# Kernel optimization log

Measured on AMD Instinct MI355X. Metric: run time of the kernel, lower is better.

Reference implementation:

```python
import jax, jax.numpy as jnp
import numpy as np

S = 192          # spatial_size
N = 100000       # active input sites
CIN, M, M2, NCLS = 3, 32, 64, 50
EPS = 1e-4       # scn BatchNorm eps
OFFS = np.array([[dx, dy, dz] for dx in (-1, 0, 1) for dy in (-1, 0, 1) for dz in (-1, 0, 1)], dtype=np.int64)


def _build_nbr(coords, size):
    # coords: [n,3] unique int64. Returns [n,27] int32 neighbor index (-1 = inactive site),
    # i.e. the submanifold-convolution rulebook built via sorted-key hashing.
    n = coords.shape[0]
    keys = (coords[:, 0] * size + coords[:, 1]) * size + coords[:, 2]
    order = np.argsort(keys)
    sk = keys[order]
    nbr = np.full((n, 27), -1, dtype=np.int32)
    for k, off in enumerate(OFFS):
        nc = coords + off
        ok = np.all((nc >= 0) & (nc < size), axis=1)
        qk = (nc[:, 0] * size + nc[:, 1]) * size + nc[:, 2]
        pos = np.searchsorted(sk, qk).clip(0, n - 1)
        hit = ok & (sk[pos] == qk)
        nbr[hit, k] = order[pos[hit]].astype(np.int32)
    return nbr


def setup_inputs() -> dict:
    rng = np.random.default_rng(0)
    raw = rng.integers(0, S, size=(130000, 3), dtype=np.int64)
    keys = (raw[:, 0] * S + raw[:, 1]) * S + raw[:, 2]
    _, first = np.unique(keys, return_index=True)
    coords = raw[np.sort(first)][:N]          # N unique active voxels
    nbr_fine = _build_nbr(coords, S)
    # stride-2 / filter-2 downsample rulebook: coarse sites = unique(coords // 2)
    S2 = S // 2
    cc = coords // 2
    ckeys = (cc[:, 0] * S2 + cc[:, 1]) * S2 + cc[:, 2]
    uk, parent = np.unique(ckeys, return_inverse=True)
    ccoords = np.column_stack((uk // (S2 * S2), (uk // S2) % S2, uk % S2))
    nbr_coarse = _build_nbr(ccoords, S2)
    offset_id = (coords[:, 0] % 2) * 4 + (coords[:, 1] % 2) * 2 + coords[:, 2] % 2
    key = jax.random.key(0)
    ks = jax.random.split(key, 8)
    def w(k, shape, fan):
        return jax.random.normal(k, shape, jnp.float32) * (1.0 / np.sqrt(fan))
    return dict(
        coords=jnp.asarray(coords, jnp.int32),
        features=jax.random.normal(ks[0], (N, CIN), jnp.float32),
        nbr_fine=jnp.asarray(nbr_fine),
        nbr_coarse=jnp.asarray(nbr_coarse),
        parent=jnp.asarray(parent.astype(np.int32)),
        offset_id=jnp.asarray(offset_id.astype(np.int32)),
        num_coarse=int(uk.shape[0]),
        w_in=w(ks[1], (27, CIN, M), 27 * CIN),
        w_b1=w(ks[2], (27, M, M), 27 * M),
        w_down=w(ks[3], (8, M, M2), 8 * M),
        w_b2=w(ks[4], (27, M2, M2), 27 * M2),
        w_up=w(ks[5], (8, M2, M), 8 * M2),
        w_b3=w(ks[6], (27, 2 * M, M), 27 * 2 * M),
        g1=jnp.ones((M,)), b1=jnp.zeros((M,)),
        gd=jnp.ones((M,)), bd=jnp.zeros((M,)),
        g2=jnp.ones((M2,)), b2=jnp.zeros((M2,)),
        gu=jnp.ones((M2,)), bu=jnp.zeros((M2,)),
        g3=jnp.ones((2 * M,)), b3=jnp.zeros((2 * M,)),
        go=jnp.ones((M,)), bo=jnp.zeros((M,)),
        w_lin=w(ks[7], (M, NCLS), M),
        b_lin=jnp.zeros((NCLS,)),
    )


def _subm_conv(f, nbr, W):
    # f: [n,Cin], nbr: [n,27] (-1 = inactive), W: [27,Cin,Cout]
    mask = nbr >= 0
    g = f[jnp.where(mask, nbr, 0)] * mask[..., None]  # [n,27,Cin]
    return jnp.einsum('nkc,kcd->nd', g, W)


def _bnrelu(f, gamma, beta):
    mu = f.mean(0)
    var = ((f - mu) ** 2).mean(0)
    return jax.nn.relu((f - mu) * (gamma / jnp.sqrt(var + EPS)) + beta)


def _down(f, parent, off_id, W, nc):
    # strided 2^3 conv: out[parent] += W[offset(child)] @ f[child]
    out = jnp.zeros((nc, W.shape[2]), f.dtype)
    for o in range(8):
        sel = (off_id == o)[:, None].astype(f.dtype)
        out = out + jax.ops.segment_sum((f * sel) @ W[o], parent, num_segments=nc)
    return out


def _up(g, parent, off_id, W):
    # 2^3 deconv back to fine sites
    gp = g[parent]
    out = jnp.zeros((gp.shape[0], W.shape[2]), g.dtype)
    for o in range(8):
        out = out + (off_id == o)[:, None].astype(g.dtype) * (gp @ W[o])
    return out


def reference(coords, features, nbr_fine, nbr_coarse, parent, offset_id, num_coarse,
              w_in, w_b1, w_down, w_b2, w_up, w_b3,
              g1, b1, gd, bd, g2, b2, gu, bu, g3, b3, go, bo, w_lin, b_lin):
    # InputLayer (coords unique -> identity) + SubmanifoldConvolution(CIN->M)
    f = _subm_conv(features, nbr_fine, w_in)
    # UNet level 0 block (pre-activation)
    f = _subm_conv(_bnrelu(f, g1, b1), nbr_fine, w_b1)
    skip = f
    # downsample: BNReLU + Convolution(M->M2, 2, 2)
    g = _down(_bnrelu(f, gd, bd), parent, offset_id, w_down, num_coarse)
    # UNet level 1 block
    g = _subm_conv(_bnrelu(g, g2, b2), nbr_coarse, w_b2)
    # upsample: BNReLU + Deconvolution(M2->M, 2, 2)
    u = _up(_bnrelu(g, gu, bu), parent, offset_id, w_up)
    # JoinTable + block (2M -> M)
    f = jnp.concatenate([skip, u], axis=1)
    f = _subm_conv(_bnrelu(f, g3, b3), nbr_fine, w_b3)
    # top-level BatchNormReLU(M) + OutputLayer + Linear head
    f = _bnrelu(f, go, bo)
    return f @ w_lin + b_lin
```

## Files before the change

### kernel.cpp

```cpp
#include <hip/hip_runtime.h>

#define EPS_BN 1e-4f
constexpr int BLK = 256;
constexpr int NCOPY = 8;

__global__ __launch_bounds__(64) void build_fine_k(
    const int* __restrict__ nbr, int n, int* __restrict__ cnt, int* __restrict__ ent) {
  int i = blockIdx.x * 64 + threadIdx.x;
  if (i >= n) return;
  int c = 0;
  const int* nr = nbr + (size_t)i * 27;
  int* er = ent + (size_t)i * 27;
#pragma unroll 1
  for (int k = 0; k < 27; ++k) {
    int j = nr[k];
    if (j >= 0) er[c++] = (k << 18) | j;
  }
  cnt[i] = c;
}

__global__ __launch_bounds__(BLK) void child_scatter_k(
    const int* __restrict__ parent, const int* __restrict__ offid, int n,
    int* __restrict__ ccnt, int* __restrict__ cent) {
  int i = blockIdx.x * BLK + threadIdx.x;
  if (i >= n) return;
  int p = parent[i];
  int slot = atomicAdd(&ccnt[p], 1);
  cent[p * 8 + slot] = i | (offid[i] << 25);
}

__global__ __launch_bounds__(BLK) void kcount_k(
    const int* __restrict__ nbr, int n, int* __restrict__ kcnt) {
  __shared__ int lc[27];
  int t = threadIdx.x;
  if (t < 27) lc[t] = 0;
  __syncthreads();
  int i = blockIdx.x * BLK + t;
  if (i < n) {
#pragma unroll 1
    for (int k = 0; k < 27; ++k)
      if (nbr[(size_t)i * 27 + k] >= 0) atomicAdd(&lc[k], 1);
  }
  __syncthreads();
  if (t < 27 && lc[t]) atomicAdd(&kcnt[t], lc[t]);
}

__global__ void kprefix_k(const int* __restrict__ kcnt,
                          int* __restrict__ segSt, int* __restrict__ kfill) {
  if (threadIdx.x == 0) {
    int s = 0;
#pragma unroll 1
    for (int k = 0; k < 27; ++k) {
      segSt[k] = s; kfill[k] = s;
      s += (kcnt[k] + 127) & ~127;
    }
    segSt[27] = s;
  }
}

__global__ __launch_bounds__(BLK) void kscatter_k(
    const int* __restrict__ nbr, int n, int* __restrict__ kfill,
    int* __restrict__ entJ, int* __restrict__ cntC, int* __restrict__ posC) {
  __shared__ int lc[27], lbase[27];
  int t = threadIdx.x;
  if (t < 27) lc[t] = 0;
  __syncthreads();
  int i = blockIdx.x * BLK + t;
  int c = 0;
  if (i < n) {
#pragma unroll 1
    for (int k = 0; k < 27; ++k) {
      if (nbr[(size_t)i * 27 + k] >= 0) { atomicAdd(&lc[k], 1); ++c; }
    }
  }
  __syncthreads();
  if (t < 27) {
    lbase[t] = lc[t] ? atomicAdd(&kfill[t], lc[t]) : 0;
    lc[t] = 0;
  }
  __syncthreads();
  if (i < n) {
    int e = 0;
#pragma unroll 1
    for (int k = 0; k < 27; ++k) {
      int j = nbr[(size_t)i * 27 + k];
      if (j >= 0) {
        int pos = lbase[k] + atomicAdd(&lc[k], 1);
        entJ[pos] = j;
        posC[(size_t)i * 27 + e] = pos;
        ++e;
      }
    }
    cntC[i] = c;
  }
}

__device__ __forceinline__ unsigned f2bf(float x) {
  unsigned u = __float_as_uint(x);
  return (u + 0x7FFFu + ((u >> 16) & 1u)) >> 16;
}

__global__ __launch_bounds__(128) void pgemm_k(
    const float* __restrict__ in, const int* __restrict__ segSt,
    const int* __restrict__ entJ,
    const float* __restrict__ sums, const float* __restrict__ gm,
    const float* __restrict__ bt, float invn,
    const float* __restrict__ W, unsigned short* __restrict__ partials) {
  __shared__ float lw[4096];
  __shared__ float lx[128 * 68];
  __shared__ float lst[128];
  int t = threadIdx.x;
  int base = blockIdx.x * 128;
  if (base >= segSt[27]) return;
  int k = 0;
#pragma unroll 1
  while (segSt[k + 1] <= base) ++k;
  if (t < 64) {
    float s = 0.f, q = 0.f;
#pragma unroll
    for (int cp = 0; cp < NCOPY; ++cp) { s += sums[cp * 128 + t]; q += sums[cp * 128 + 64 + t]; }
    float mu = s * invn, var = q * invn - mu * mu;
    float sc = gm[t] / sqrtf(var + EPS_BN);
    lst[t] = sc; lst[64 + t] = bt[t] - mu * sc;
  }
  const float4* wsrc = reinterpret_cast<const float4*>(W + (size_t)k * 4096);
#pragma unroll
  for (int q = 0; q < 8; ++q)
    reinterpret_cast<float4*>(lw)[t + q * 128] = wsrc[t + q * 128];
  __syncthreads();
#pragma unroll 1
  for (int it = 0; it < 16; ++it) {
    int idx = t + it * 128;
    int pr = idx >> 4, cq = idx & 15;
    int j = entJ[base + pr];
    float4 x = *reinterpret_cast<const float4*>(in + (size_t)j * 64 + cq * 4);
    int cb = cq * 4;
    float y0 = fmaf(x.x, lst[cb + 0], lst[64 + cb + 0]);
    float y1 = fmaf(x.y, lst[cb + 1], lst[64 + cb + 1]);
    float y2 = fmaf(x.z, lst[cb + 2], lst[64 + cb + 2]);
    float y3 = fmaf(x.w, lst[cb + 3], lst[64 + cb + 3]);
    *reinterpret_cast<float4*>(&lx[pr * 68 + cb]) =
        make_float4(y0 > 0.f ? y0 : 0.f, y1 > 0.f ? y1 : 0.f,
                    y2 > 0.f ? y2 : 0.f, y3 > 0.f ? y3 : 0.f);
  }
  __syncthreads();
  int slot = t >> 3, g = (t & 7) * 8;
  float acc[8][8];
#pragma unroll
  for (int pp = 0; pp < 8; ++pp)
#pragma unroll
    for (int b = 0; b < 8; ++b) acc[pp][b] = 0.f;
#pragma unroll
  for (int c4 = 0; c4 < 16; ++c4) {
    int cb = c4 * 4;
    float4 xq[8];
#pragma unroll
    for (int pp = 0; pp < 8; ++pp)
      xq[pp] = *reinterpret_cast<const float4*>(&lx[(slot + 16 * pp) * 68 + cb]);
#pragma unroll
    for (int q = 0; q < 4; ++q) {
      float4 wa = *reinterpret_cast<const float4*>(&lw[(cb + q) * 64 + g]);
      float4 wb = *reinterpret_cast<const float4*>(&lw[(cb + q) * 64 + g + 4]);
      float ws[8] = {wa.x, wa.y, wa.z, wa.w, wb.x, wb.y, wb.z, wb.w};
#pragma unroll
      for (int pp = 0; pp < 8; ++pp) {
        float xv = q == 0 ? xq[pp].x : (q == 1 ? xq[pp].y : (q == 2 ? xq[pp].z : xq[pp].w));
#pragma unroll
        for (int b = 0; b < 8; ++b) acc[pp][b] = fmaf(xv, ws[b], acc[pp][b]);
      }
    }
  }
#pragma unroll
  for (int pp = 0; pp < 8; ++pp) {
    int p = base + slot + 16 * pp;
    uint4 o;
    o.x = f2bf(acc[pp][0]) | (f2bf(acc[pp][1]) << 16);
    o.y = f2bf(acc[pp][2]) | (f2bf(acc[pp][3]) << 16);
    o.z = f2bf(acc[pp][4]) | (f2bf(acc[pp][5]) << 16);
    o.w = f2bf(acc[pp][6]) | (f2bf(acc[pp][7]) << 16);
    *reinterpret_cast<uint4*>(partials + ((size_t)p * 64 + g)) = o;
  }
}

__global__ __launch_bounds__(BLK) void pgather_k(
    const unsigned short* __restrict__ partials, const int* __restrict__ cntC,
    const int* __restrict__ posC, float* __restrict__ out, int nc,
    float* __restrict__ osums) {
  __shared__ float red[256];
  int t = threadIdx.x;
  for (int idx = t; idx < 256; idx += BLK) red[idx] = 0.f;
  __syncthreads();
  int slot = t >> 4, g = (t & 15) * 4;
  int row = blockIdx.x * 16 + slot;
  float a0 = 0.f, a1 = 0.f, a2 = 0.f, a3 = 0.f;
  if (row < nc) {
    int c = cntC[row];
    const int* pr = posC + (size_t)row * 27;
#pragma unroll 1
    for (int e = 0; e < c; ++e) {
      int pos = pr[e];
      uint2 u = *reinterpret_cast<const uint2*>(partials + ((size_t)pos * 64 + g));
      a0 += __uint_as_float(u.x << 16);
      a1 += __uint_as_float(u.x & 0xFFFF0000u);
      a2 += __uint_as_float(u.y << 16);
      a3 += __uint_as_float(u.y & 0xFFFF0000u);
    }
    *reinterpret_cast<float4*>(out + (size_t)row * 64 + g) = make_float4(a0, a1, a2, a3);
  }
  atomicAdd(&red[g + 0], a0); atomicAdd(&red[g + 1], a1);
  atomicAdd(&red[g + 2], a2); atomicAdd(&red[g + 3], a3);
  atomicAdd(&red[128 + g + 0], a0 * a0); atomicAdd(&red[128 + g + 1], a1 * a1);
  atomicAdd(&red[128 + g + 2], a2 * a2); atomicAdd(&red[128 + g + 3], a3 * a3);
  __syncthreads();
  int copy = blockIdx.x & (NCOPY - 1);
  if (t < 128) {
    int half = t >> 6, ch = t & 63;
    atomicAdd(&osums[copy * 128 + half * 64 + ch], red[half * 128 + ch]);
  }
}

template <int CI, int CO, int MODE>
__global__ __launch_bounds__(BLK) void tconvA_k(
    const float* __restrict__ in, const int* __restrict__ ent, const int* __restrict__ cnt,
    const int* __restrict__ parent, const int* __restrict__ offid,
    const float* __restrict__ W, float* __restrict__ out, int n,
    float* __restrict__ osums) {
  constexpr int LANES = CO / 4, SLOTS = BLK / LANES, RPS = 64 / SLOTS;
  __shared__ float red[2 * CO];
  int t = threadIdx.x;
  for (int idx = t; idx < 2 * CO; idx += BLK) red[idx] = 0.f;
  __syncthreads();
  int slot = t / LANES, lane = t % LANES, g = lane * 4;
  int T = blockIdx.x;
  float ssum[4] = {0, 0, 0, 0}, ssq[4] = {0, 0, 0, 0};
#pragma unroll 1
  for (int rr = 0; rr < RPS; ++rr) {
    int row = T * 64 + slot * RPS + rr;
    bool vrow = row < n;
    float a0 = 0.f, a1 = 0.f, a2 = 0.f, a3 = 0.f;
    int ec = 0;
    if (vrow) ec = (MODE == 2) ? 1 : cnt[row];
#pragma unroll 1
    for (int e = 0; e < ec; ++e) {
      int k, j;
      if constexpr (MODE == 0) {
        int v = ent[(size_t)row * 27 + e];
        k = (v >> 18) & 31; j = v & 0x3FFFF;
      } else if constexpr (MODE == 1) {
        int v = ent[(size_t)row * 8 + e];
        k = v >> 25; j = v & 0x1FFFFFF;
      } else {
        k = offid[row]; j = parent[row];
      }
      const float* Wk = W + (size_t)k * (CI * CO) + g;
      const float* xr = in + (size_t)j * CI;
#pragma unroll
      for (int h = 0; h < CI / 32; ++h) {
        float4 xv[8];
#pragma unroll
        for (int c4 = 0; c4 < 8; ++c4)
          xv[c4] = *reinterpret_cast<const float4*>(xr + h * 32 + c4 * 4);
#pragma unroll
        for (int c4 = 0; c4 < 8; ++c4) {
          float xs[4] = {xv[c4].x, xv[c4].y, xv[c4].z, xv[c4].w};
#pragma unroll
          for (int q = 0; q < 4; ++q) {
            float4 wv = *reinterpret_cast<const float4*>(Wk + (size_t)(h * 32 + c4 * 4 + q) * CO);
            a0 = fmaf(xs[q], wv.x, a0);
            a1 = fmaf(xs[q], wv.y, a1);
            a2 = fmaf(xs[q], wv.z, a2);
            a3 = fmaf(xs[q], wv.w, a3);
          }
        }
      }
    }
    if (vrow)
      *reinterpret_cast<float4*>(out + (size_t)row * CO + g) = make_float4(a0, a1, a2, a3);
    ssum[0] += a0; ssum[1] += a1; ssum[2] += a2; ssum[3] += a3;
    ssq[0] = fmaf(a0, a0, ssq[0]); ssq[1] = fmaf(a1, a1, ssq[1]);
    ssq[2] = fmaf(a2, a2, ssq[2]); ssq[3] = fmaf(a3, a3, ssq[3]);
  }
#pragma unroll
  for (int q = 0; q < 4; ++q) {
    atomicAdd(&red[g + q], ssum[q]);
    atomicAdd(&red[CO + g + q], ssq[q]);
  }
  __syncthreads();
  int copy = blockIdx.x & (NCOPY - 1);
  if (t < 2 * CO) atomicAdd(&osums[copy * 2 * CO + t], red[t]);
}

template <int C>
__global__ __launch_bounds__(BLK) void bnact_k(
    const float* __restrict__ in, const float* __restrict__ sums,
    const float* __restrict__ gm, const float* __restrict__ bt, float invn,
    float* __restrict__ outp, int n) {
  __shared__ float lst[2 * C];
  int t = threadIdx.x;
  if (t < C) {
    float s = 0.f, q = 0.f;
#pragma unroll
    for (int cp = 0; cp < NCOPY; ++cp) { s += sums[cp * 2 * C + t]; q += sums[cp * 2 * C + C + t]; }
    float mu = s * invn, var = q * invn - mu * mu;
    float sc = gm[t] / sqrtf(var + EPS_BN);
    lst[t] = sc; lst[C + t] = bt[t] - mu * sc;
  }
  __syncthreads();
  int total = n * (C / 4);
  const float4* in4 = reinterpret_cast<const float4*>(in);
  float4* out4 = reinterpret_cast<float4*>(outp);
  for (int idx = blockIdx.x * BLK + t; idx < total; idx += gridDim.x * BLK) {
    int cb = (idx & (C / 4 - 1)) * 4;
    float4 x = in4[idx];
    float v[4] = {x.x, x.y, x.z, x.w};
#pragma unroll
    for (int q = 0; q < 4; ++q) {
      float y = fmaf(v[q], lst[cb + q], lst[C + cb + q]);
      v[q] = y > 0.f ? y : 0.f;
    }
    out4[idx] = make_float4(v[0], v[1], v[2], v[3]);
  }
}

__global__ __launch_bounds__(BLK) void bncat_k(
    const float* __restrict__ fa, const float* __restrict__ sA,
    const float* __restrict__ gA, const float* __restrict__ bA,
    const float* __restrict__ fb, const float* __restrict__ sB,
    const float* __restrict__ gB, const float* __restrict__ bB,
    float invn, float* __restrict__ acat, int n) {
  __shared__ float lst[128];
  int t = threadIdx.x;
  if (t < 64) {
    int half = t >> 5, c = t & 31;
    const float* ss = half ? sB : sA;
    const float* gg = half ? gB : gA;
    const float* bb = half ? bB : bA;
    float s = 0.f, q = 0.f;
#pragma unroll
    for (int cp = 0; cp < NCOPY; ++cp) { s += ss[cp * 64 + c]; q += ss[cp * 64 + 32 + c]; }
    float mu = s * invn, var = q * invn - mu * mu;
    float sc = gg[c] / sqrtf(var + EPS_BN);
    lst[half * 64 + c] = sc; lst[half * 64 + 32 + c] = bb[c] - mu * sc;
  }
  __syncthreads();
  int total = n * 16;
  for (int idx = blockIdx.x * BLK + t; idx < total; idx += gridDim.x * BLK) {
    int row = idx >> 4, c4 = idx & 15;
    int half = c4 >> 3, cc = (c4 & 7) * 4;
    const float* src = half ? fb : fa;
    float4 x = *reinterpret_cast<const float4*>(src + (size_t)row * 32 + cc);
    const float* L = lst + half * 64;
    float v[4] = {x.x, x.y, x.z, x.w};
#pragma unroll
    for (int q = 0; q < 4; ++q) {
      float y = fmaf(v[q], L[cc + q], L[32 + cc + q]);
      v[q] = y > 0.f ? y : 0.f;
    }
    *reinterpret_cast<float4*>(acat + (size_t)row * 64 + c4 * 4) = make_float4(v[0], v[1], v[2], v[3]);
  }
}

__global__ __launch_bounds__(BLK) void conv_in_k(
    const float* __restrict__ feat, const int* __restrict__ nbr,
    const float* __restrict__ W, float* __restrict__ out, int n,
    float* __restrict__ osums) {
  int i = blockIdx.x * BLK + threadIdx.x;
  bool valid = i < n;
  float acc[32];
#pragma unroll
  for (int c = 0; c < 32; ++c) acc[c] = 0.f;
#pragma unroll 1
  for (int k = 0; k < 27; ++k) {
    int j = valid ? nbr[(size_t)i * 27 + k] : -1;
    if (j < 0) continue;
    float x0 = feat[j * 3 + 0], x1 = feat[j * 3 + 1], x2 = feat[j * 3 + 2];
    const float* w0 = W + k * 96;
#pragma unroll
    for (int co = 0; co < 8; ++co) {
      float4 a = *reinterpret_cast<const float4*>(w0 + co * 4);
      float4 b = *reinterpret_cast<const float4*>(w0 + 32 + co * 4);
      float4 cc = *reinterpret_cast<const float4*>(w0 + 64 + co * 4);
      acc[4*co+0] = fmaf(x0, a.x, fmaf(x1, b.x, fmaf(x2, cc.x, acc[4*co+0])));
      acc[4*co+1] = fmaf(x0, a.y, fmaf(x1, b.y, fmaf(x2, cc.y, acc[4*co+1])));
      acc[4*co+2] = fmaf(x0, a.z, fmaf(x1, b.z, fmaf(x2, cc.z, acc[4*co+2])));
      acc[4*co+3] = fmaf(x0, a.w, fmaf(x1, b.w, fmaf(x2, cc.w, acc[4*co+3])));
    }
  }
  if (valid) {
    float* o = out + (size_t)i * 32;
#pragma unroll
    for (int co = 0; co < 8; ++co)
      *reinterpret_cast<float4*>(o + co * 4) = make_float4(acc[4*co], acc[4*co+1], acc[4*co+2], acc[4*co+3]);
  }
  __shared__ float red[2][4][32];
  int w = threadIdx.x >> 6;
#pragma unroll
  for (int c = 0; c < 32; ++c) {
    float v = acc[c], q = acc[c] * acc[c];
#pragma unroll
    for (int off = 32; off; off >>= 1) {
      v += __shfl_down(v, off);
      q += __shfl_down(q, off);
    }
    if ((threadIdx.x & 63) == 0) { red[0][w][c] = v; red[1][w][c] = q; }
  }
  __syncthreads();
  if (threadIdx.x < 64) {
    int kind = threadIdx.x >> 5, c = threadIdx.x & 31;
    float s = red[kind][0][c] + red[kind][1][c] + red[kind][2][c] + red[kind][3][c];
    atomicAdd(&osums[(blockIdx.x & (NCOPY - 1)) * 64 + kind * 32 + c], s);
  }
}

__global__ __launch_bounds__(BLK) void head_k(
    const float* __restrict__ fin, const float* __restrict__ sums,
    const float* __restrict__ gm, const float* __restrict__ bt, float inv_n,
    const float* __restrict__ Wl, const float* __restrict__ bl,
    float* __restrict__ out, int n) {
  __shared__ float lw[32 * 50];
  __shared__ float lb[52];
  __shared__ float lst[64];
  int t = threadIdx.x;
  if (t < 32) {
    float s = 0.f, q = 0.f;
#pragma unroll
    for (int cp = 0; cp < NCOPY; ++cp) { s += sums[cp * 64 + t]; q += sums[cp * 64 + 32 + t]; }
    float mu = s * inv_n, var = q * inv_n - mu * mu;
    float sc = gm[t] / sqrtf(var + EPS_BN);
    lst[t] = sc; lst[32 + t] = bt[t] - mu * sc;
  }
  for (int idx = t; idx < 1600; idx += BLK) lw[idx] = Wl[idx];
  if (t < 50) lb[t] = bl[t];
  __syncthreads();
  int i = blockIdx.x * BLK + t;
  if (i >= n) return;
  float x[32];
  const float* fj = fin + (size_t)i * 32;
#pragma unroll
  for (int c4 = 0; c4 < 8; ++c4) {
    float4 v = *reinterpret_cast<const float4*>(fj + c4 * 4);
    float vs[4] = {v.x, v.y, v.z, v.w};
#pragma unroll
    for (int q = 0; q < 4; ++q) {
      int c = c4 * 4 + q;
      float y = fmaf(vs[q], lst[c], lst[32 + c]);
      x[c] = y > 0.f ? y : 0.f;
    }
  }
  float acc[50];
#pragma unroll
  for (int co = 0; co < 50; ++co) acc[co] = lb[co];
#pragma unroll 4
  for (int c = 0; c < 32; ++c) {
#pragma unroll
    for (int co = 0; co < 50; ++co) acc[co] = fmaf(x[c], lw[c * 50 + co], acc[co]);
  }
  float* o = out + (size_t)i * 50;
#pragma unroll
  for (int co = 0; co < 25; ++co)
    *reinterpret_cast<float2*>(o + co * 2) = make_float2(acc[co * 2], acc[co * 2 + 1]);
}

extern "C" void kernel_launch(void* const* d_in, const int* in_sizes, int n_in,
                              void* d_out, int out_size, void* d_ws, size_t ws_size,
                              hipStream_t stream) {
  const float* feat   = (const float*)d_in[1];
  const int*   nbrF   = (const int*)d_in[2];
  const int*   nbrC   = (const int*)d_in[3];
  const int*   parent = (const int*)d_in[4];
  const int*   offid  = (const int*)d_in[5];
  const float* w_in   = (const float*)d_in[7];
  const float* w_b1   = (const float*)d_in[8];
  const float* w_down = (const float*)d_in[9];
  const float* w_b2   = (const float*)d_in[10];
  const float* w_up   = (const float*)d_in[11];
  const float* w_b3   = (const float*)d_in[12];
  const float* g1v = (const float*)d_in[13], *b1v = (const float*)d_in[14];
  const float* gdv = (const float*)d_in[15], *bdv = (const float*)d_in[16];
  const float* g2v = (const float*)d_in[17], *b2v = (const float*)d_in[18];
  const float* guv = (const float*)d_in[19], *buv = (const float*)d_in[20];
  const float* g3v = (const float*)d_in[21], *b3v = (const float*)d_in[22];
  const float* gov = (const float*)d_in[23], *bov = (const float*)d_in[24];
  const float* w_lin = (const float*)d_in[25];
  const float* b_lin = (const float*)d_in[26];
  float* out = (float*)d_out;

  int N  = in_sizes[4];
  int NC = in_sizes[3] / 27;
  int ntF = (N + 63) / 64, ntC = (NC + 63) / 64;
  int CAPP = ((NC * 9 / 2) / 128 + 28) * 128;

  size_t szF = (size_t)N * 32;
  size_t szG = (size_t)NC * 64;
  size_t SB  = (size_t)N * 64;

  float* ws = (float*)d_ws;
  float* S1 = ws;
  float* S2 = S1 + SB;
  float* S3 = S2 + SB;
  float* S4 = S3 + szF;
  float* S5 = S4 + szF;
  float* sums1 = S5 + szG;
  float* sumsD = sums1 + 8 * 64;
  float* sums2 = sumsD + 8 * 64;
  float* sumsU = sums2 + 8 * 128;
  float* sums4 = sumsU + 8 * 128;
  float* sums5 = sums4 + 8 * 64;
  int* ccnt = (int*)(sums5 + 8 * 64);
  int* cent = ccnt + NC;
  int* cntF = cent + (size_t)NC * 8;
  int* entF = cntF + N;
  int* kcnt = entF + (size_t)N * 27;
  int* segSt = kcnt + 32;
  int* kfill = segSt + 32;
  int* cntC = kfill + 32;
  int* posC = cntC + NC;
  int* entJ = posC + (size_t)NC * 27;
  unsigned short* partials = (unsigned short*)
      (((uintptr_t)(entJ + CAPP) + 15) & ~(uintptr_t)15);

  hipMemsetAsync(sums1, 0, (4096 + NC) * sizeof(float), stream);
  hipMemsetAsync(kcnt, 0, 96 * sizeof(int), stream);
  hipMemsetAsync(entJ, 0, (size_t)CAPP * sizeof(int), stream);

  int gridN = (N + BLK - 1) / BLK;
  int gridC = (NC + BLK - 1) / BLK;
  int agrid = 1024;
  float invN = 1.f / (float)N, invC = 1.f / (float)NC;

  build_fine_k<<<ntF, 64, 0, stream>>>(nbrF, N, cntF, entF);
  child_scatter_k<<<gridN, BLK, 0, stream>>>(parent, offid, N, ccnt, cent);
  kcount_k<<<gridC, BLK, 0, stream>>>(nbrC, NC, kcnt);
  kprefix_k<<<1, 32, 0, stream>>>(kcnt, segSt, kfill);
  kscatter_k<<<gridC, BLK, 0, stream>>>(nbrC, NC, kfill, entJ, cntC, posC);

  conv_in_k<<<gridN, BLK, 0, stream>>>(feat, nbrF, w_in, S1, N, sums1);
  bnact_k<32><<<agrid, BLK, 0, stream>>>(S1, sums1, g1v, b1v, invN, S2, N);

  tconvA_k<32, 32, 0><<<ntF, BLK, 0, stream>>>(
      S2, entF, cntF, nullptr, nullptr, w_b1, S3, N, sumsD);
  bnact_k<32><<<agrid, BLK, 0, stream>>>(S3, sumsD, gdv, bdv, invN, S4, N);

  tconvA_k<32, 64, 1><<<ntC, BLK, 0, stream>>>(
      S4, cent, ccnt, nullptr, nullptr, w_down, S5, NC, sums2);

  int gridP1 = CAPP / 128;
  pgemm_k<<<gridP1, 128, 0, stream>>>(
      S5, segSt, entJ, sums2, g2v, b2v, invC, w_b2, partials);
  pgather_k<<<(NC + 15) / 16, BLK, 0, stream>>>(
      partials, cntC, posC, S1, NC, sumsU);

  bnact_k<64><<<agrid, BLK, 0, stream>>>(S1, sumsU, guv, buv, invC, S5, NC);

  tconvA_k<64, 32, 2><<<ntF, BLK, 0, stream>>>(
      S5, nullptr, nullptr, parent, offid, w_up, S4, N, sums4);

  bncat_k<<<agrid, BLK, 0, stream>>>(
      S3, sumsD, g3v, b3v, S4, sums4, g3v + 32, b3v + 32, invN, S2, N);

  tconvA_k<64, 32, 0><<<ntF, BLK, 0, stream>>>(
      S2, entF, cntF, nullptr, nullptr, w_b3, S3, N, sums5);

  head_k<<<gridN, BLK, 0, stream>>>(S3, sums5, gov, bov, invN, w_lin, b_lin, out, N);
}
```

Measured before the change: 527.4 us.

## Use per-offset gather-GEMM-scatter for fine submanifold convolutions with fused BN and concat

Both fine-level submanifold convolutions (w_b1 and w_b3) now use the offset-grouped rulebook path that previously served only the coarse conv. Entries are grouped by kernel offset, each group runs a dense GEMM against one shared-memory weight slice, and a gather kernel sums fp32 partials per output row. The BN+ReLU that used to run as separate bnact and bncat passes is folded into the GEMM input load, and the concat is read directly from two source buffers. This replaces per-row atomic-style convolution with more reuse of the weights, but adds fine rulebook build kernels and a large fp32 partials round trip.

```diff
diff --git a/kernel.cpp b/kernel.cpp
--- a/kernel.cpp
+++ b/kernel.cpp
@@ -3,21 +3,6 @@
 #define EPS_BN 1e-4f
 constexpr int BLK = 256;
 constexpr int NCOPY = 8;
-
-__global__ __launch_bounds__(64) void build_fine_k(
-    const int* __restrict__ nbr, int n, int* __restrict__ cnt, int* __restrict__ ent) {
-  int i = blockIdx.x * 64 + threadIdx.x;
-  if (i >= n) return;
-  int c = 0;
-  const int* nr = nbr + (size_t)i * 27;
-  int* er = ent + (size_t)i * 27;
-#pragma unroll 1
-  for (int k = 0; k < 27; ++k) {
-    int j = nr[k];
-    if (j >= 0) er[c++] = (k << 18) | j;
-  }
-  cnt[i] = c;
-}
 
 __global__ __launch_bounds__(BLK) void child_scatter_k(
     const int* __restrict__ parent, const int* __restrict__ offid, int n,
@@ -60,7 +45,7 @@
 
 __global__ __launch_bounds__(BLK) void kscatter_k(
     const int* __restrict__ nbr, int n, int* __restrict__ kfill,
-    int* __restrict__ entJ, int* __restrict__ cntC, int* __restrict__ posC) {
+    int* __restrict__ entJ, int* __restrict__ cntR, int* __restrict__ posR) {
   __shared__ int lc[27], lbase[27];
   int t = threadIdx.x;
   if (t < 27) lc[t] = 0;
@@ -69,9 +54,8 @@
   int c = 0;
   if (i < n) {
 #pragma unroll 1
-    for (int k = 0; k < 27; ++k) {
+    for (int k = 0; k < 27; ++k)
       if (nbr[(size_t)i * 27 + k] >= 0) { atomicAdd(&lc[k], 1); ++c; }
-    }
   }
   __syncthreads();
   if (t < 27) {
@@ -87,11 +71,11 @@
       if (j >= 0) {
         int pos = lbase[k] + atomicAdd(&lc[k], 1);
         entJ[pos] = j;
-        posC[(size_t)i * 27 + e] = pos;
+        posR[(size_t)i * 27 + e] = pos;
         ++e;
       }
     }
-    cntC[i] = c;
+    cntR[i] = c;
   }
 }
 
@@ -100,70 +84,88 @@
   return (u + 0x7FFFu + ((u >> 16) & 1u)) >> 16;
 }
 
+template <int CI, int CO, bool CAT, bool BF>
 __global__ __launch_bounds__(128) void pgemm_k(
-    const float* __restrict__ in, const int* __restrict__ segSt,
-    const int* __restrict__ entJ,
-    const float* __restrict__ sums, const float* __restrict__ gm,
-    const float* __restrict__ bt, float invn,
-    const float* __restrict__ W, unsigned short* __restrict__ partials) {
-  __shared__ float lw[4096];
-  __shared__ float lx[128 * 68];
-  __shared__ float lst[128];
+    const float* __restrict__ inA, const float* __restrict__ inB,
+    const int* __restrict__ segSt, const int* __restrict__ entJ,
+    const float* __restrict__ sumsA, const float* __restrict__ gmA,
+    const float* __restrict__ btA, float invA,
+    const float* __restrict__ sumsB, const float* __restrict__ gmB,
+    const float* __restrict__ btB, float invB,
+    const float* __restrict__ W, void* __restrict__ partials) {
+  constexpr int XP = CI + 4;
+  constexpr int C4 = CI / 4;
+  constexpr int NS = 1024 / CO;
+  constexpr int PP = 128 / NS;
+  constexpr int CIA = CAT ? CI / 2 : CI;
+  constexpr int WL = CI * CO / 512;
+  __shared__ float lw[CI * CO];
+  __shared__ float lx[128 * XP];
+  __shared__ float lst[2 * CI];
   int t = threadIdx.x;
   int base = blockIdx.x * 128;
   if (base >= segSt[27]) return;
   int k = 0;
 #pragma unroll 1
   while (segSt[k + 1] <= base) ++k;
-  if (t < 64) {
+  if (t < CI) {
+    const float* S; const float* G; const float* B; float inv; int c;
+    if (!CAT || t < CIA) { S = sumsA; G = gmA; B = btA; inv = invA; c = t; }
+    else { S = sumsB; G = gmB; B = btB; inv = invB; c = t - CIA; }
     float s = 0.f, q = 0.f;
 #pragma unroll
-    for (int cp = 0; cp < NCOPY; ++cp) { s += sums[cp * 128 + t]; q += sums[cp * 128 + 64 + t]; }
-    float mu = s * invn, var = q * invn - mu * mu;
-    float sc = gm[t] / sqrtf(var + EPS_BN);
-    lst[t] = sc; lst[64 + t] = bt[t] - mu * sc;
-  }
-  const float4* wsrc = reinterpret_cast<const float4*>(W + (size_t)k * 4096);
-#pragma unroll
-  for (int q = 0; q < 8; ++q)
+    for (int cp = 0; cp < NCOPY; ++cp) { s += S[cp * 2 * CIA + c]; q += S[cp * 2 * CIA + CIA + c]; }
+    float mu = s * inv, var = q * inv - mu * mu;
+    float sc = G[c] / sqrtf(var + EPS_BN);
+    lst[t] = sc; lst[CI + t] = B[c] - mu * sc;
+  }
+  const float4* wsrc = reinterpret_cast<const float4*>(W + (size_t)k * (CI * CO));
+#pragma unroll
+  for (int q = 0; q < WL; ++q)
     reinterpret_cast<float4*>(lw)[t + q * 128] = wsrc[t + q * 128];
   __syncthreads();
 #pragma unroll 1
-  for (int it = 0; it < 16; ++it) {
+  for (int it = 0; it < C4; ++it) {
     int idx = t + it * 128;
-    int pr = idx >> 4, cq = idx & 15;
+    int pr = idx / C4, cq = idx % C4;
     int j = entJ[base + pr];
-    float4 x = *reinterpret_cast<const float4*>(in + (size_t)j * 64 + cq * 4);
     int cb = cq * 4;
-    float y0 = fmaf(x.x, lst[cb + 0], lst[64 + cb + 0]);
-    float y1 = fmaf(x.y, lst[cb + 1], lst[64 + cb + 1]);
-    float y2 = fmaf(x.z, lst[cb + 2], lst[64 + cb + 2]);
-    float y3 = fmaf(x.w, lst[cb + 3], lst[64 + cb + 3]);
-    *reinterpret_cast<float4*>(&lx[pr * 68 + cb]) =
+    float4 x;
+    if constexpr (CAT) {
+      x = (cb < CIA) ? *reinterpret_cast<const float4*>(inA + (size_t)j * CIA + cb)
+                     : *reinterpret_cast<const float4*>(inB + (size_t)j * CIA + (cb - CIA));
+    } else {
+      x = *reinterpret_cast<const float4*>(inA + (size_t)j * CI + cb);
+    }
+    float y0 = fmaf(x.x, lst[cb + 0], lst[CI + cb + 0]);
+    float y1 = fmaf(x.y, lst[cb + 1], lst[CI + cb + 1]);
+    float y2 = fmaf(x.z, lst[cb + 2], lst[CI + cb + 2]);
+    float y3 = fmaf(x.w, lst[cb + 3], lst[CI + cb + 3]);
+    *reinterpret_cast<float4*>(&lx[pr * XP + cb]) =
         make_float4(y0 > 0.f ? y0 : 0.f, y1 > 0.f ? y1 : 0.f,
                     y2 > 0.f ? y2 : 0.f, y3 > 0.f ? y3 : 0.f);
   }
   __syncthreads();
-  int slot = t >> 3, g = (t & 7) * 8;
-  float acc[8][8];
-#pragma unroll
-  for (int pp = 0; pp < 8; ++pp)
+  int slot = t / PP, g = (t % PP) * 8;
+  float acc[PP][8];
+#pragma unroll
+  for (int pp = 0; pp < PP; ++pp)
 #pragma unroll
     for (int b = 0; b < 8; ++b) acc[pp][b] = 0.f;
 #pragma unroll
-  for (int c4 = 0; c4 < 16; ++c4) {
+  for (int c4 = 0; c4 < C4; ++c4) {
     int cb = c4 * 4;
-    float4 xq[8];
-#pragma unroll
-    for (int pp = 0; pp < 8; ++pp)
-      xq[pp] = *reinterpret_cast<const float4*>(&lx[(slot + 16 * pp) * 68 + cb]);
+    float4 xq[PP];
+#pragma unroll
+    for (int pp = 0; pp < PP; ++pp)
+      xq[pp] = *reinterpret_cast<const float4*>(&lx[(slot + NS * pp) * XP + cb]);
 #pragma unroll
     for (int q = 0; q < 4; ++q) {
-      float4 wa = *reinterpret_cast<const float4*>(&lw[(cb + q) * 64 + g]);
-      float4 wb = *reinterpret_cast<const float4*>(&lw[(cb + q) * 64 + g + 4]);
+      float4 wa = *reinterpret_cast<const float4*>(&lw[(cb + q) * CO + g]);
+      float4 wb = *reinterpret_cast<const float4*>(&lw[(cb + q) * CO + g + 4]);
       float ws[8] = {wa.x, wa.y, wa.z, wa.w, wb.x, wb.y, wb.z, wb.w};
 #pragma unroll
-      for (int pp = 0; pp < 8; ++pp) {
+      for (int pp = 0; pp < PP; ++pp) {
         float xv = q == 0 ? xq[pp].x : (q == 1 ? xq[pp].y : (q == 2 ? xq[pp].z : xq[pp].w));
 #pragma unroll
         for (int b = 0; b < 8; ++b) acc[pp][b] = fmaf(xv, ws[b], acc[pp][b]);
@@ -171,52 +173,62 @@
     }
   }
 #pragma unroll
-  for (int pp = 0; pp < 8; ++pp) {
-    int p = base + slot + 16 * pp;
-    uint4 o;
-    o.x = f2bf(acc[pp][0]) | (f2bf(acc[pp][1]) << 16);
-    o.y = f2bf(acc[pp][2]) | (f2bf(acc[pp][3]) << 16);
-    o.z = f2bf(acc[pp][4]) | (f2bf(acc[pp][5]) << 16);
-    o.w = f2bf(acc[pp][6]) | (f2bf(acc[pp][7]) << 16);
-    *reinterpret_cast<uint4*>(partials + ((size_t)p * 64 + g)) = o;
-  }
-}
-
+  for (int pp = 0; pp < PP; ++pp) {
+    size_t p = base + slot + NS * pp;
+    if constexpr (BF) {
+      uint4 o;
+      o.x = f2bf(acc[pp][0]) | (f2bf(acc[pp][1]) << 16);
+      o.y = f2bf(acc[pp][2]) | (f2bf(acc[pp][3]) << 16);
+      o.z = f2bf(acc[pp][4]) | (f2bf(acc[pp][5]) << 16);
+      o.w = f2bf(acc[pp][6]) | (f2bf(acc[pp][7]) << 16);
+      *reinterpret_cast<uint4*>((unsigned short*)partials + p * CO + g) = o;
+    } else {
+      float* pf = (float*)partials + p * CO + g;
+      *reinterpret_cast<float4*>(pf) = make_float4(acc[pp][0], acc[pp][1], acc[pp][2], acc[pp][3]);
+      *reinterpret_cast<float4*>(pf + 4) = make_float4(acc[pp][4], acc[pp][5], acc[pp][6], acc[pp][7]);
+    }
+  }
+}
+
+template <int CO, bool BF>
 __global__ __launch_bounds__(BLK) void pgather_k(
-    const unsigned short* __restrict__ partials, const int* __restrict__ cntC,
-    const int* __restrict__ posC, float* __restrict__ out, int nc,
+    const void* __restrict__ partials, const int* __restrict__ cntR,
+    const int* __restrict__ posR, float* __restrict__ out, int n,
     float* __restrict__ osums) {
-  __shared__ float red[256];
-  int t = threadIdx.x;
-  for (int idx = t; idx < 256; idx += BLK) red[idx] = 0.f;
-  __syncthreads();
-  int slot = t >> 4, g = (t & 15) * 4;
-  int row = blockIdx.x * 16 + slot;
+  constexpr int LPS = CO / 4, RPB = BLK / LPS;
+  __shared__ float red[2 * CO];
+  int t = threadIdx.x;
+  for (int idx = t; idx < 2 * CO; idx += BLK) red[idx] = 0.f;
+  __syncthreads();
+  int slot = t / LPS, g = (t % LPS) * 4;
+  int row = blockIdx.x * RPB + slot;
   float a0 = 0.f, a1 = 0.f, a2 = 0.f, a3 = 0.f;
-  if (row < nc) {
-    int c = cntC[row];
-    const int* pr = posC + (size_t)row * 27;
+  if (row < n) {
+    int c = cntR[row];
+    const int* pr = posR + (size_t)row * 27;
 #pragma unroll 1
     for (int e = 0; e < c; ++e) {
-      int pos = pr[e];
-      uint2 u = *reinterpret_cast<const uint2*>(partials + ((size_t)pos * 64 + g));
-      a0 += __uint_as_float(u.x << 16);
-      a1 += __uint_as_float(u.x & 0xFFFF0000u);
-      a2 += __uint_as_float(u.y << 16);
-      a3 += __uint_as_float(u.y & 0xFFFF0000u);
-    }
-    *reinterpret_cast<float4*>(out + (size_t)row * 64 + g) = make_float4(a0, a1, a2, a3);
+      size_t pos = (size_t)pr[e];
+      if constexpr (BF) {
+        uint2 u = *reinterpret_cast<const uint2*>((const unsigned short*)partials + pos * CO + g);
+        a0 += __uint_as_float(u.x << 16);
+        a1 += __uint_as_float(u.x & 0xFFFF0000u);
+        a2 += __uint_as_float(u.y << 16);
+        a3 += __uint_as_float(u.y & 0xFFFF0000u);
+      } else {
+        float4 v = *reinterpret_cast<const float4*>((const float*)partials + pos * CO + g);
+        a0 += v.x; a1 += v.y; a2 += v.z; a3 += v.w;
+      }
+    }
+    *reinterpret_cast<float4*>(out + (size_t)row * CO + g) = make_float4(a0, a1, a2, a3);
   }
   atomicAdd(&red[g + 0], a0); atomicAdd(&red[g + 1], a1);
   atomicAdd(&red[g + 2], a2); atomicAdd(&red[g + 3], a3);
-  atomicAdd(&red[128 + g + 0], a0 * a0); atomicAdd(&red[128 + g + 1], a1 * a1);
-  atomicAdd(&red[128 + g + 2], a2 * a2); atomicAdd(&red[128 + g + 3], a3 * a3);
+  atomicAdd(&red[CO + g + 0], a0 * a0); atomicAdd(&red[CO + g + 1], a1 * a1);
+  atomicAdd(&red[CO + g + 2], a2 * a2); atomicAdd(&red[CO + g + 3], a3 * a3);
   __syncthreads();
   int copy = blockIdx.x & (NCOPY - 1);
-  if (t < 128) {
-    int half = t >> 6, ch = t & 63;
-    atomicAdd(&osums[copy * 128 + half * 64 + ch], red[half * 128 + ch]);
-  }
+  if (t < 2 * CO) atomicAdd(&osums[copy * 2 * CO + t], red[t]);
 }
 
 template <int CI, int CO, int MODE>
@@ -243,10 +255,7 @@
 #pragma unroll 1
     for (int e = 0; e < ec; ++e) {
       int k, j;
-      if constexpr (MODE == 0) {
-        int v = ent[(size_t)row * 27 + e];
-        k = (v >> 18) & 31; j = v & 0x3FFFF;
-      } else if constexpr (MODE == 1) {
+      if constexpr (MODE == 1) {
         int v = ent[(size_t)row * 8 + e];
         k = v >> 25; j = v & 0x1FFFFFF;
       } else {
@@ -319,44 +328,6 @@
       v[q] = y > 0.f ? y : 0.f;
     }
     out4[idx] = make_float4(v[0], v[1], v[2], v[3]);
-  }
-}
-
-__global__ __launch_bounds__(BLK) void bncat_k(
-    const float* __restrict__ fa, const float* __restrict__ sA,
-    const float* __restrict__ gA, const float* __restrict__ bA,
-    const float* __restrict__ fb, const float* __restrict__ sB,
-    const float* __restrict__ gB, const float* __restrict__ bB,
-    float invn, float* __restrict__ acat, int n) {
-  __shared__ float lst[128];
-  int t = threadIdx.x;
-  if (t < 64) {
-    int half = t >> 5, c = t & 31;
-    const float* ss = half ? sB : sA;
-    const float* gg = half ? gB : gA;
-    const float* bb = half ? bB : bA;
-    float s = 0.f, q = 0.f;
-#pragma unroll
-    for (int cp = 0; cp < NCOPY; ++cp) { s += ss[cp * 64 + c]; q += ss[cp * 64 + 32 + c]; }
-    float mu = s * invn, var = q * invn - mu * mu;
-    float sc = gg[c] / sqrtf(var + EPS_BN);
-    lst[half * 64 + c] = sc; lst[half * 64 + 32 + c] = bb[c] - mu * sc;
-  }
-  __syncthreads();
-  int total = n * 16;
-  for (int idx = blockIdx.x * BLK + t; idx < total; idx += gridDim.x * BLK) {
-    int row = idx >> 4, c4 = idx & 15;
-    int half = c4 >> 3, cc = (c4 & 7) * 4;
-    const float* src = half ? fb : fa;
-    float4 x = *reinterpret_cast<const float4*>(src + (size_t)row * 32 + cc);
-    const float* L = lst + half * 64;
-    float v[4] = {x.x, x.y, x.z, x.w};
-#pragma unroll
-    for (int q = 0; q < 4; ++q) {
-      float y = fmaf(v[q], L[cc + q], L[32 + cc + q]);
-      v[q] = y > 0.f ? y : 0.f;
-    }
-    *reinterpret_cast<float4*>(acat + (size_t)row * 64 + c4 * 4) = make_float4(v[0], v[1], v[2], v[3]);
   }
 }
 
@@ -488,78 +459,81 @@
   int N  = in_sizes[4];
   int NC = in_sizes[3] / 27;
   int ntF = (N + 63) / 64, ntC = (NC + 63) / 64;
-  int CAPP = ((NC * 9 / 2) / 128 + 28) * 128;
-
-  size_t szF = (size_t)N * 32;
-  size_t szG = (size_t)NC * 64;
-  size_t SB  = (size_t)N * 64;
+  int CAPPF = ((N * 3) / 128 + 28) * 128;
+  int CAPPC = ((NC * 9 / 2) / 128 + 28) * 128;
 
   float* ws = (float*)d_ws;
-  float* S1 = ws;
-  float* S2 = S1 + SB;
-  float* S3 = S2 + SB;
-  float* S4 = S3 + szF;
-  float* S5 = S4 + szF;
-  float* sums1 = S5 + szG;
+  float* B1 = ws;
+  float* B2 = B1 + (size_t)N * 32;
+  float* B3 = B2 + (size_t)N * 32;
+  float* B4 = B3 + (size_t)N * 32;
+  float* B5 = B4 + (size_t)NC * 64;
+  float* sums1 = B5 + (size_t)NC * 64;
   float* sumsD = sums1 + 8 * 64;
   float* sums2 = sumsD + 8 * 64;
   float* sumsU = sums2 + 8 * 128;
   float* sums4 = sumsU + 8 * 128;
   float* sums5 = sums4 + 8 * 64;
   int* ccnt = (int*)(sums5 + 8 * 64);
-  int* cent = ccnt + NC;
+  int* kcntF = ccnt + NC;
+  int* kcntC = kcntF + 32;
+  int* segStF = kcntC + 32;
+  int* kfillF = segStF + 32;
+  int* segStC = kfillF + 32;
+  int* kfillC = segStC + 32;
+  int* cent = kfillC + 32;
   int* cntF = cent + (size_t)NC * 8;
-  int* entF = cntF + N;
-  int* kcnt = entF + (size_t)N * 27;
-  int* segSt = kcnt + 32;
-  int* kfill = segSt + 32;
-  int* cntC = kfill + 32;
+  int* posF = cntF + N;
+  int* cntC = posF + (size_t)N * 27;
   int* posC = cntC + NC;
-  int* entJ = posC + (size_t)NC * 27;
-  unsigned short* partials = (unsigned short*)
-      (((uintptr_t)(entJ + CAPP) + 15) & ~(uintptr_t)15);
-
-  hipMemsetAsync(sums1, 0, (4096 + NC) * sizeof(float), stream);
-  hipMemsetAsync(kcnt, 0, 96 * sizeof(int), stream);
-  hipMemsetAsync(entJ, 0, (size_t)CAPP * sizeof(int), stream);
+  int* entJF = posC + (size_t)NC * 27;
+  int* entJC = entJF + CAPPF;
+  float* partialsF = (float*)(((uintptr_t)(entJC + CAPPC) + 15) & ~(uintptr_t)15);
+  unsigned short* partialsC = (unsigned short*)(partialsF + (size_t)CAPPF * 32);
+
+  hipMemsetAsync(sums1, 0, (4096 + NC + 64) * sizeof(float), stream);
+  hipMemsetAsync(entJF, 0, (size_t)(CAPPF + CAPPC) * sizeof(int), stream);
 
   int gridN = (N + BLK - 1) / BLK;
   int gridC = (NC + BLK - 1) / BLK;
   int agrid = 1024;
   float invN = 1.f / (float)N, invC = 1.f / (float)NC;
 
-  build_fine_k<<<ntF, 64, 0, stream>>>(nbrF, N, cntF, entF);
+  kcount_k<<<gridN, BLK, 0, stream>>>(nbrF, N, kcntF);
+  kcount_k<<<gridC, BLK, 0, stream>>>(nbrC, NC, kcntC);
+  kprefix_k<<<1, 32, 0, stream>>>(kcntF, segStF, kfillF);
+  kprefix_k<<<1, 32, 0, stream>>>(kcntC, segStC, kfillC);
+  kscatter_k<<<gridN, BLK, 0, stream>>>(nbrF, N, kfillF, entJF, cntF, posF);
+  kscatter_k<<<gridC, BLK, 0, stream>>>(nbrC, NC, kfillC, entJC, cntC, posC);
   child_scatter_k<<<gridN, BLK, 0, stream>>>(parent, offid, N, ccnt, cent);
-  kcount_k<<<gridC, BLK, 0, stream>>>(nbrC, NC, kcnt);
-  kprefix_k<<<1, 32, 0, stream>>>(kcnt, segSt, kfill);
-  kscatter_k<<<gridC, BLK, 0, stream>>>(nbrC, NC, kfill, entJ, cntC, posC);
-
-  conv_in_k<<<gridN, BLK, 0, stream>>>(feat, nbrF, w_in, S1, N, sums1);
-  bnact_k<32><<<agrid, BLK, 0, stream>>>(S1, sums1, g1v, b1v, invN, S2, N);
-
-  tconvA_k<32, 32, 0><<<ntF, BLK, 0, stream>>>(
-      S2, entF, cntF, nullptr, nullptr, w_b1, S3, N, sumsD);
-  bnact_k<32><<<agrid, BLK, 0, stream>>>(S3, sumsD, gdv, bdv, invN, S4, N);
+
+  conv_in_k<<<gridN, BLK, 0, stream>>>(feat, nbrF, w_in, B1, N, sums1);
+
+  pgemm_k<32, 32, false, false><<<CAPPF / 128, 128, 0, stream>>>(
+      B1, nullptr, segStF, entJF, sums1, g1v, b1v, invN,
+      nullptr, nullptr, nullptr, 0.f, w_b1, partialsF);
+  pgather_k<32, false><<<(N + 31) / 32, BLK, 0, stream>>>(
+      partialsF, cntF, posF, B2, N, sumsD);
+  bnact_k<32><<<agrid, BLK, 0, stream>>>(B2, sumsD, gdv, bdv, invN, B3, N);
 
   tconvA_k<32, 64, 1><<<ntC, BLK, 0, stream>>>(
-      S4, cent, ccnt, nullptr, nullptr, w_down, S5, NC, sums2);
-
-  int gridP1 = CAPP / 128;
-  pgemm_k<<<gridP1, 128, 0, stream>>>(
-      S5, segSt, entJ, sums2, g2v, b2v, invC, w_b2, partials);
-  pgather_k<<<(NC + 15) / 16, BLK, 0, stream>>>(
-      partials, cntC, posC, S1, NC, sumsU);
-
-  bnact_k<64><<<agrid, BLK, 0, stream>>>(S1, sumsU, guv, buv, invC, S5, NC);
+      B3, cent, ccnt, nullptr, nullptr, w_down, B4, NC, sums2);
+
+  pgemm_k<64, 64, false, true><<<CAPPC / 128, 128, 0, stream>>>(
+      B4, nullptr, segStC, entJC, sums2, g2v, b2v, invC,
+      nullptr, nullptr, nullptr, 0.f, w_b2, partialsC);
+  pgather_k<64, true><<<(NC + 15) / 16, BLK, 0, stream>>>(
+      partialsC, cntC, posC, B4, NC, sumsU);
+  bnact_k<64><<<agrid, BLK, 0, stream>>>(B4, sumsU, guv, buv, invC, B5, NC);
 
   tconvA_k<64, 32, 2><<<ntF, BLK, 0, stream>>>(
-      S5, nullptr, nullptr, parent, offid, w_up, S4, N, sums4);
-
-  bncat_k<<<agrid, BLK, 0, stream>>>(
-      S3, sumsD, g3v, b3v, S4, sums4, g3v + 32, b3v + 32, invN, S2, N);
-
-  tconvA_k<64, 32, 0><<<ntF, BLK, 0, stream>>>(
-      S2, entF, cntF, nullptr, nullptr, w_b3, S3, N, sums5);
-
-  head_k<<<gridN, BLK, 0, stream>>>(S3, sums5, gov, bov, invN, w_lin, b_lin, out, N);
-}
+      B5, nullptr, nullptr, parent, offid, w_up, B1, N, sums4);
+
+  pgemm_k<64, 32, true, false><<<CAPPF / 128, 128, 0, stream>>>(
+      B2, B1, segStF, entJF, sumsD, g3v, b3v, invN,
+      sums4, g3v + 32, b3v + 32, invN, w_b3, partialsF);
+  pgather_k<32, false><<<(N + 31) / 32, BLK, 0, stream>>>(
+      partialsF, cntF, posF, B3, N, sums5);
+
+  head_k<<<gridN, BLK, 0, stream>>>(B3, sums5, gov, bov, invN, w_lin, b_lin, out, N);
+}
```

New measurement: 518.6 us. About the same (-1.7%).
